# Performance work log

Measured on AMD Instinct MI355X. Metric: run time of the kernel, lower is better.

The kernel has to match this reference:

```python
import jax, jax.numpy as jnp
import numpy as np
from functools import partial


def deform_sample(inp, dy, dx):
    """Bilinear sample inp[b,c] at (y+dy[b,c,y,x], x+dx[b,c,y,x]) with zero padding.
    inp, dy, dx: [B, C, H, W] -> [B, C, H, W]. Matches torchvision deform_conv2d
    with 1x1 kernel and offset_groups == C (one offset pair per channel)."""
    B, C, H, W = inp.shape
    ys = jnp.arange(H, dtype=inp.dtype)[None, None, :, None] + dy  # [B,C,H,W]
    xs = jnp.arange(W, dtype=inp.dtype)[None, None, None, :] + dx
    y0f = jnp.floor(ys)
    x0f = jnp.floor(xs)
    wy = ys - y0f
    wx = xs - x0f
    y0 = y0f.astype(jnp.int32)
    x0 = x0f.astype(jnp.int32)
    flat = inp.reshape(B, C, H * W)

    def gather(yi, xi):
        valid = (yi >= 0) & (yi < H) & (xi >= 0) & (xi < W)
        idx = jnp.clip(yi, 0, H - 1) * W + jnp.clip(xi, 0, W - 1)
        v = jnp.take_along_axis(flat, idx.reshape(B, C, H * W), axis=2).reshape(B, C, H, W)
        return jnp.where(valid, v, jnp.zeros((), inp.dtype))

    return ((1 - wy) * (1 - wx) * gather(y0, x0)
            + (1 - wy) * wx * gather(y0, x0 + 1)
            + wy * (1 - wx) * gather(y0 + 1, x0)
            + wy * wx * gather(y0 + 1, x0 + 1))


def atm_layer(x, offset, w_weight, w_bias, h_weight, h_bias, local_weight, local_bias,
              fc1_w, fc1_b, fc2_w, fc2_b, proj_w, proj_b):
    B, H, W, C = x.shape
    x_nchw = jnp.transpose(x, (0, 3, 1, 2))  # [B,C,H,W]
    zeros = jnp.zeros_like(x_nchw)

    # ATM along w: offset[:, :C] is x-offset (offset_t[:,1::2]), y-offset 0
    sw = deform_sample(x_nchw, zeros, offset[:, :C])
    w = jnp.einsum('bchw,oc->bhwo', sw, w_weight) + w_bias  # [B,H,W,C]

    # ATM along h: offset[:, C:] is y-offset (offset_t[:,0::2]), x-offset 0
    sh = deform_sample(x_nchw, offset[:, C:], zeros)
    h = jnp.einsum('bchw,oc->bhwo', sh, h_weight) + h_bias

    # depthwise 5x5 conv, padding 2
    c = jax.lax.conv_general_dilated(
        x_nchw, local_weight, window_strides=(1, 1), padding=((2, 2), (2, 2)),
        feature_group_count=C, dimension_numbers=('NCHW', 'OIHW', 'NCHW'))
    c = jnp.transpose(c, (0, 2, 3, 1)) + local_bias  # [B,H,W,C]

    # gating MLP: global average -> fc1 -> GELU -> fc2 -> softmax over 3 branches
    a = (w + h + c).mean(axis=(1, 2))  # [B,C]
    a = jax.nn.gelu(a @ fc1_w.T + fc1_b, approximate=False)
    a = a @ fc2_w.T + fc2_b  # [B,3C]
    a = jnp.transpose(a.reshape(B, C, 3), (2, 0, 1))  # [3,B,C]
    a = jax.nn.softmax(a, axis=0)[:, :, None, None, :]  # [3,B,1,1,C]

    out = w * a[0] + h * a[1] + c * a[2]
    out = out @ proj_w.T + proj_b
    return out


def setup_inputs() -> dict:
    C = 256
    B, H, W = 16, 64, 64
    key = jax.random.key(0)
    ks = jax.random.split(key, 16)
    bnd = 1.0 / np.sqrt(C)
    hid = C // 4
    return {
        'x': jax.random.normal(ks[0], (B, H, W, C), jnp.float32),
        'offset': jax.random.normal(ks[1], (B, 2 * C, H, W), jnp.float32),
        'w_weight': jax.random.uniform(ks[2], (C, C), jnp.float32, -bnd, bnd),
        'w_bias': jax.random.uniform(ks[3], (C,), jnp.float32, -bnd, bnd),
        'h_weight': jax.random.uniform(ks[4], (C, C), jnp.float32, -bnd, bnd),
        'h_bias': jax.random.uniform(ks[5], (C,), jnp.float32, -bnd, bnd),
        'local_weight': jax.random.uniform(ks[6], (C, 1, 5, 5), jnp.float32, -0.2, 0.2),
        'local_bias': jax.random.uniform(ks[7], (C,), jnp.float32, -0.2, 0.2),
        'fc1_w': jax.random.uniform(ks[8], (hid, C), jnp.float32, -bnd, bnd),
        'fc1_b': jax.random.uniform(ks[9], (hid,), jnp.float32, -bnd, bnd),
        'fc2_w': jax.random.uniform(ks[10], (3 * C, hid), jnp.float32, -1.0 / np.sqrt(hid), 1.0 / np.sqrt(hid)),
        'fc2_b': jax.random.uniform(ks[11], (3 * C,), jnp.float32, -1.0 / np.sqrt(hid), 1.0 / np.sqrt(hid)),
        'proj_w': jax.random.uniform(ks[12], (C, C), jnp.float32, -bnd, bnd),
        'proj_b': jax.random.uniform(ks[13], (C,), jnp.float32, -bnd, bnd),
    }


def reference(x, offset, w_weight, w_bias, h_weight, h_bias, local_weight, local_bias,
              fc1_w, fc1_b, fc2_w, fc2_b, proj_w, proj_b):
    return atm_layer(x, offset, w_weight, w_bias, h_weight, h_bias, local_weight,
                     local_bias, fc1_w, fc1_b, fc2_w, fc2_b, proj_w, proj_b)
```

## Files before the change

kernel.cpp:

```cpp
#include <hip/hip_runtime.h>
#include <hip/hip_bf16.h>

typedef _Float16 half4_t __attribute__((ext_vector_type(4)));
typedef _Float16 half8 __attribute__((ext_vector_type(8)));
typedef float f32x4 __attribute__((ext_vector_type(4)));

#define BB 16
#define HH 64
#define WW2 64
#define CC 256

__global__ __launch_bounds__(256) void k_pre(
    const float* __restrict__ Ww, const float* __restrict__ Wh,
    const float* __restrict__ pw,
    _Float16* __restrict__ WwT, _Float16* __restrict__ WhT,
    _Float16* __restrict__ pf, float* __restrict__ sums)
{
  __shared__ _Float16 tile[64][65];
  const int blk = blockIdx.x;
  const int t = threadIdx.x;

  if (blk < 32) {
    const int nt = blk & 3, kt = (blk >> 2) & 3, mat = blk >> 4;
    const float* src = mat ? Wh : Ww;
    _Float16* dst = mat ? WhT : WwT;
    const int n0 = nt * 64, k0 = kt * 64;
    const int sl = t & 63;
    #pragma unroll
    for (int p = 0; p < 16; p++) {
      int chl = (t >> 6) + p * 4;
      tile[chl][sl] = (_Float16)src[(size_t)(n0 + chl) * 256 + k0 + sl];
    }
    __syncthreads();
    #pragma unroll
    for (int p = 0; p < 2; p++) {
      int pl = (t >> 3) + p * 32;
      int c8 = (t & 7) * 8;
      half8 hv;
      #pragma unroll
      for (int r = 0; r < 8; r++) hv[r] = tile[c8 + r][pl];
      *(half8*)(dst + (size_t)(k0 + pl) * 256 + n0 + c8) = hv;
    }
  } else if (blk < 80) {
    sums[(blk - 32) * 256 + t] = 0.f;
  } else {
    int i = (blk - 80) * 2048 + t * 8;
    float4 v0 = *(const float4*)(pw + i);
    float4 v1 = *(const float4*)(pw + i + 4);
    half8 h = {(_Float16)v0.x, (_Float16)v0.y, (_Float16)v0.z, (_Float16)v0.w,
               (_Float16)v1.x, (_Float16)v1.y, (_Float16)v1.z, (_Float16)v1.w};
    *(half8*)(pf + i) = h;
  }
}

__global__ __launch_bounds__(256) void k_transA(
    const float* __restrict__ x, const float* __restrict__ off,
    _Float16* __restrict__ swb, float* __restrict__ ssw)
{
  __shared__ _Float16 tile[64][65];
  __shared__ _Float16 xr[64][68];
  __shared__ float red[4][64];

  const int work = (blockIdx.x & 7) * 512 + (blockIdx.x >> 3);
  const int st   = work & 63;
  const int cht  = (work >> 6) & 3;
  const int b    = work >> 8;
  const int t = threadIdx.x;

  const int ch0 = cht * 64;
  const float* src = off + ((size_t)b * 512 + ch0) * 4096 + st * 64;
  const int sl = t & 63;
  #pragma unroll
  for (int p = 0; p < 16; p++) {
    int chl = (t >> 6) + p * 4;
    tile[chl][sl] = (_Float16)src[(size_t)chl * 4096 + sl];
  }

  const float* xs_src = x + ((size_t)(b * 64 + st) * 64) * 256 + ch0;
  const int xrow = t >> 2;
  const int c16 = (t & 3) * 16;
  #pragma unroll
  for (int j = 0; j < 4; j++) {
    float4 v = *(const float4*)(xs_src + (size_t)xrow * 256 + c16 + j * 4);
    half4_t h = {(_Float16)v.x, (_Float16)v.y, (_Float16)v.z, (_Float16)v.w};
    *(half4_t*)(&xr[xrow][c16 + j * 4]) = h;
  }
  __syncthreads();

  const int cl = t & 63, xg = t >> 6;
  const int cg = ch0 + cl;
  _Float16* sp = swb + ((size_t)(b * 64 + st) * 64) * 256 + cg;
  float asw = 0.f;
  #pragma unroll
  for (int k = 0; k < 16; k++) {
    int xi = xg * 16 + k;
    float dx = (float)tile[cl][xi];
    float xs2 = (float)xi + dx;
    float xf = floorf(xs2);
    float wx = xs2 - xf;
    int xq = (int)xf;
    float v0 = (xq >= 0 && xq < 64) ? (float)xr[xq][cl] : 0.f;
    float v1 = (xq + 1 >= 0 && xq + 1 < 64) ? (float)xr[xq + 1][cl] : 0.f;
    float swv = (1.f - wx) * v0 + wx * v1;
    sp[(size_t)xi * 256] = (_Float16)swv;
    asw += swv;
  }
  red[xg][cl] = asw;
  __syncthreads();
  if (t < 64)
    atomicAdd(&ssw[b * CC + ch0 + t],
              red[0][t] + red[1][t] + red[2][t] + red[3][t]);
}

__global__ __launch_bounds__(256) void k_transB(const float* __restrict__ off,
                                                _Float16* __restrict__ offBT)
{
  __shared__ _Float16 tile[64][65];
  const int work = (blockIdx.x & 7) * 512 + (blockIdx.x >> 3);
  const int st   = work & 63;
  const int cht  = (work >> 6) & 3;
  const int b    = work >> 8;
  const int t = threadIdx.x;

  const int ch0 = 256 + cht * 64;
  const float* src = off + ((size_t)b * 512 + ch0) * 4096 + st * 64;
  const int sl = t & 63;
  #pragma unroll
  for (int p = 0; p < 16; p++) {
    int chl = (t >> 6) + p * 4;
    tile[chl][sl] = (_Float16)src[(size_t)chl * 4096 + sl];
  }
  __syncthreads();

  #pragma unroll
  for (int p = 0; p < 2; p++) {
    int pl = (t >> 3) + p * 32;
    int c8 = (t & 7) * 8;
    half8 hv;
    #pragma unroll
    for (int r = 0; r < 8; r++) hv[r] = tile[c8 + r][pl];
    int s = st * 64 + pl;
    size_t pix = (size_t)b * 4096 + (s & 63) * 64 + (s >> 6);
    *(half8*)(offBT + pix * 256 + cht * 64 + c8) = hv;
  }
}

__global__ __launch_bounds__(256) void k_conv(
    const float* __restrict__ x, const float* __restrict__ lw,
    _Float16* __restrict__ cvb, float* __restrict__ scv)
{
  const int work = (blockIdx.x & 7) * 256 + (blockIdx.x >> 3);
  const int xh = work & 1;
  const int y  = (work >> 1) & 63;
  const int b  = work >> 7;
  const int c = threadIdx.x;

  float wgt[25];
  #pragma unroll
  for (int q = 0; q < 25; q++) wgt[q] = lw[c * 25 + q];

  const float* xb = x + (size_t)b * HH * WW2 * CC + c;
  const float* rp[5];
  bool yv[5];
  #pragma unroll
  for (int ky = 0; ky < 5; ky++) {
    int yy = y + ky - 2;
    yv[ky] = (yy >= 0 && yy < HH);
    rp[ky] = xb + (size_t)(yv[ky] ? yy : 0) * WW2 * CC;
  }

  _Float16* cp = cvb + ((size_t)b * 4096 + y * 64) * CC + c;
  float acv = 0.f;
  const int x0 = xh * 32;

  for (int g = 0; g < 4; ++g) {
    const int u0 = x0 + g * 8;
    float col[60];
    #pragma unroll
    for (int j = 0; j < 12; j++) {
      int xx = u0 + j - 2;
      bool xv = (xx >= 0 && xx < 64);
      int xxc = xv ? xx : 0;
      #pragma unroll
      for (int ky = 0; ky < 5; ky++) {
        float v = rp[ky][(size_t)xxc * CC];
        col[j * 5 + ky] = (xv && yv[ky]) ? v : 0.f;
      }
    }
    #pragma unroll
    for (int o = 0; o < 8; o++) {
      float cv = 0.f;
      #pragma unroll
      for (int kx = 0; kx < 5; kx++) {
        const int j5 = (o + kx) * 5;
        cv += wgt[0 + kx]  * col[j5 + 0] + wgt[5 + kx]  * col[j5 + 1] +
              wgt[10 + kx] * col[j5 + 2] + wgt[15 + kx] * col[j5 + 3] +
              wgt[20 + kx] * col[j5 + 4];
      }
      cp[(size_t)(u0 + o) * CC] = (_Float16)cv;
      acv += cv;
    }
  }
  atomicAdd(&scv[b * CC + c], acv);
}

__global__ __launch_bounds__(256) void k_col(
    const float* __restrict__ x, const _Float16* __restrict__ offBT,
    _Float16* __restrict__ shb, float* __restrict__ ssh)
{
  __shared__ _Float16 xc[64 * 128];
  const int work = (blockIdx.x & 7) * 256 + (blockIdx.x >> 3);
  const int ch = work & 1;
  const int xi = (work >> 1) & 63;
  const int b  = work >> 7;
  const int ch0 = ch * 128;
  const int t = threadIdx.x;

  #pragma unroll
  for (int p = 0; p < 4; p++) {
    int i = p * 2048 + t * 8;
    int yy = i >> 7, cl = i & 127;
    const float* s = x + ((size_t)(b * 64 + yy) * 64 + xi) * 256 + ch0 + cl;
    float4 v0 = *(const float4*)(s);
    float4 v1 = *(const float4*)(s + 4);
    half8 h = {(_Float16)v0.x, (_Float16)v0.y, (_Float16)v0.z, (_Float16)v0.w,
               (_Float16)v1.x, (_Float16)v1.y, (_Float16)v1.z, (_Float16)v1.w};
    *(half8*)(xc + i) = h;
  }
  __syncthreads();

  const int cl = t & 127, yg = t >> 7;
  const _Float16* obt = offBT + ((size_t)(b * 64 + xi) * 64) * 256 + ch0 + cl;
  _Float16* hp = shb + ((size_t)(b * 64) * 64 + xi) * 256 + ch0 + cl;
  float ash = 0.f;
  #pragma unroll 8
  for (int k = 0; k < 32; k++) {
    int yy = yg * 32 + k;
    float dy = (float)obt[(size_t)yy * 256];
    float ys = (float)yy + dy;
    float yf = floorf(ys);
    float wy = ys - yf;
    int yq = (int)yf;
    float u0 = (yq >= 0 && yq < 64) ? (float)xc[yq * 128 + cl] : 0.f;
    float u1 = (yq + 1 >= 0 && yq + 1 < 64) ? (float)xc[(yq + 1) * 128 + cl] : 0.f;
    float shv = (1.f - wy) * u0 + wy * u1;
    hp[(size_t)yy * 64 * 256] = (_Float16)shv;
    ash += shv;
  }
  atomicAdd(&ssh[b * CC + ch0 + cl], ash);
}

__global__ __launch_bounds__(256) void k_gate(
    const float* __restrict__ ssw, const float* __restrict__ ssh, const float* __restrict__ scv,
    const float* __restrict__ Ww, const float* __restrict__ bw,
    const float* __restrict__ Wh, const float* __restrict__ bh,
    const float* __restrict__ blc,
    const float* __restrict__ fc1w, const float* __restrict__ fc1b,
    const float* __restrict__ fc2w, const float* __restrict__ fc2b,
    _Float16* __restrict__ gh, float* __restrict__ bcomb)
{
  __shared__ float sswl[CC], sshl[CC], avgl[CC], tl[64];
  const int b = blockIdx.x, tid = threadIdx.x;
  sswl[tid] = ssw[b * CC + tid];
  sshl[tid] = ssh[b * CC + tid];
  __syncthreads();

  float acc = scv[b * CC + tid];
  for (int c = 0; c < CC; c++)
    acc += sswl[c] * Ww[tid * CC + c] + sshl[c] * Wh[tid * CC + c];
  avgl[tid] = acc * (1.f / (HH * WW2)) + bw[tid] + bh[tid] + blc[tid];
  __syncthreads();

  if (tid < 64) {
    float a = fc1b[tid];
    for (int o = 0; o < CC; o++) a += avgl[o] * fc1w[tid * CC + o];
    tl[tid] = 0.5f * a * (1.f + erff(a * 0.70710678118654752f));
  }
  __syncthreads();

  float g[3];
  #pragma unroll
  for (int j = 0; j < 3; j++) {
    float a = fc2b[tid * 3 + j];
    for (int k = 0; k < 64; k++) a += tl[k] * fc2w[(tid * 3 + j) * 64 + k];
    g[j] = a;
  }
  float m = fmaxf(g[0], fmaxf(g[1], g[2]));
  float e0 = expf(g[0] - m), e1 = expf(g[1] - m), e2 = expf(g[2] - m);
  float inv = 1.f / (e0 + e1 + e2);
  float a0 = e0 * inv, a1 = e1 * inv, a2 = e2 * inv;
  gh[(0 * BB + b) * CC + tid] = (_Float16)a0;
  gh[(1 * BB + b) * CC + tid] = (_Float16)a1;
  gh[(2 * BB + b) * CC + tid] = (_Float16)a2;
  bcomb[b * CC + tid] = a0 * bw[tid] + a1 * bh[tid] + a2 * blc[tid];
}

__global__ __launch_bounds__(256) void k_mats(
    const _Float16* __restrict__ pf, const _Float16* __restrict__ gh,
    const _Float16* __restrict__ WwT, const _Float16* __restrict__ WhT,
    const float* __restrict__ bcomb, const float* __restrict__ pb,
    _Float16* __restrict__ Bcat, float* __restrict__ bias_out)
{
  const int blk = (blockIdx.x & 7) * 16 + (blockIdx.x >> 3);
  const int ob = blk & 3;
  const int br = (blk >> 2) & 1;
  const int b  = blk >> 3;
  const int o0 = ob * 64;
  const int tid = threadIdx.x;
  const int wid = tid >> 6, l = tid & 63;
  const int n0 = wid * 64;
  const int lr = l & 15;
  const int kg = (l >> 4) * 8;
  const int jr = (l >> 4) * 4;

  const _Float16* WT  = br ? WhT : WwT;
  const _Float16* ghb = gh + (size_t)(br * BB + b) * CC;

  f32x4 acc[4][4];
  #pragma unroll
  for (int mi = 0; mi < 4; mi++)
    #pragma unroll
    for (int ni = 0; ni < 4; ni++) acc[mi][ni] = (f32x4){0.f, 0.f, 0.f, 0.f};

  #pragma unroll
  for (int ks = 0; ks < 8; ks++) {
    half8 gv = *(const half8*)(ghb + kg + ks * 32);
    half8 a[4], bbv[4];
    #pragma unroll
    for (int mi = 0; mi < 4; mi++)
      a[mi] = *(const half8*)(pf + (size_t)(o0 + mi * 16 + lr) * CC + kg + ks * 32) * gv;
    #pragma unroll
    for (int ni = 0; ni < 4; ni++)
      bbv[ni] = *(const half8*)(WT + (size_t)(n0 + ni * 16 + lr) * CC + kg + ks * 32);
    #pragma unroll
    for (int mi = 0; mi < 4; mi++)
      #pragma unroll
      for (int ni = 0; ni < 4; ni++)
        acc[mi][ni] = __builtin_amdgcn_mfma_f32_16x16x32_f16(a[mi], bbv[ni], acc[mi][ni], 0, 0, 0);
  }

  #pragma unroll
  for (int ni = 0; ni < 4; ni++) {
    int kcol = n0 + ni * 16 + lr;
    #pragma unroll
    for (int mi = 0; mi < 4; mi++) {
      #pragma unroll
      for (int j = 0; j < 4; j++) {
        int o = o0 + mi * 16 + jr + j;
        Bcat[((size_t)b * CC + o) * 512 + br * 256 + kcol] = (_Float16)acc[mi][ni][j];
      }
    }
  }

  if (br == 0) {
    int o_l = tid >> 2, part = tid & 3;
    const _Float16* pr = pf + (size_t)(o0 + o_l) * CC + part * 64;
    const float* bc = bcomb + b * CC + part * 64;
    float s = 0.f;
    #pragma unroll
    for (int i = 0; i < 8; i++) {
      half8 h = *(const half8*)(pr + i * 8);
      #pragma unroll
      for (int r = 0; r < 8; r++) s += (float)h[r] * bc[i * 8 + r];
    }
    s += __shfl_xor(s, 1);
    s += __shfl_xor(s, 2);
    if (part == 0) bias_out[b * CC + o0 + o_l] = s + pb[o0 + o_l];
  }
}

#define APAD 264
__global__ __launch_bounds__(256) void k_gemm(
    const _Float16* __restrict__ swb, const _Float16* __restrict__ shb,
    const _Float16* __restrict__ cvb, const _Float16* __restrict__ Bcat,
    const _Float16* __restrict__ pf, const _Float16* __restrict__ a2h,
    const float* __restrict__ bias_out, float* __restrict__ out)
{
  __shared__ _Float16 smem[64 * APAD];

  const int work = (blockIdx.x & 7) * 128 + (blockIdx.x >> 3);
  const int r0 = work * 64;
  const int b = work >> 6;
  const int tid = threadIdx.x;
  const int wid = tid >> 6, l = tid & 63;
  const int n0 = wid * 64;
  const int lr = l & 15;
  const int kg = (l >> 4) * 8;
  const int jr = (l >> 4) * 4;

  const _Float16* bq = Bcat + ((size_t)b * CC + n0 + lr) * 512 + kg;

  f32x4 acc[4][4];
  #pragma unroll
  for (int mi = 0; mi < 4; mi++)
    #pragma unroll
    for (int ni = 0; ni < 4; ni++) acc[mi][ni] = (f32x4){0.f, 0.f, 0.f, 0.f};

  half8 st[8];
  {
    const _Float16* g = swb + (size_t)r0 * CC;
    #pragma unroll
    for (int p = 0; p < 8; p++) st[p] = *(const half8*)(g + p * 2048 + tid * 8);
    #pragma unroll
    for (int p = 0; p < 8; p++) {
      int i = p * 2048 + tid * 8;
      *(half8*)(smem + (i >> 8) * APAD + (i & 255)) = st[p];
    }
  }
  __syncthreads();
  {
    const _Float16* g = shb + (size_t)r0 * CC;
    #pragma unroll
    for (int p = 0; p < 8; p++) st[p] = *(const half8*)(g + p * 2048 + tid * 8);
  }
  #pragma unroll
  for (int ks = 0; ks < 8; ks++) {
    half8 a[4], bbv[4];
    #pragma unroll
    for (int mi = 0; mi < 4; mi++)
      a[mi] = *(const half8*)(smem + (mi * 16 + lr) * APAD + kg + ks * 32);
    #pragma unroll
    for (int ni = 0; ni < 4; ni++)
      bbv[ni] = *(const half8*)(bq + (size_t)ni * 16 * 512 + ks * 32);
    #pragma unroll
    for (int mi = 0; mi < 4; mi++)
      #pragma unroll
      for (int ni = 0; ni < 4; ni++)
        acc[mi][ni] = __builtin_amdgcn_mfma_f32_16x16x32_f16(a[mi], bbv[ni], acc[mi][ni], 0, 0, 0);
  }
  __syncthreads();
  #pragma unroll
  for (int p = 0; p < 8; p++) {
    int i = p * 2048 + tid * 8;
    *(half8*)(smem + (i >> 8) * APAD + (i & 255)) = st[p];
  }
  __syncthreads();
  {
    const _Float16* g = cvb + (size_t)r0 * CC;
    #pragma unroll
    for (int p = 0; p < 8; p++) st[p] = *(const half8*)(g + p * 2048 + tid * 8);
  }
  #pragma unroll
  for (int ks = 0; ks < 8; ks++) {
    half8 a[4], bbv[4];
    #pragma unroll
    for (int mi = 0; mi < 4; mi++)
      a[mi] = *(const half8*)(smem + (mi * 16 + lr) * APAD + kg + ks * 32);
    #pragma unroll
    for (int ni = 0; ni < 4; ni++)
      bbv[ni] = *(const half8*)(bq + (size_t)ni * 16 * 512 + 256 + ks * 32);
    #pragma unroll
    for (int mi = 0; mi < 4; mi++)
      #pragma unroll
      for (int ni = 0; ni < 4; ni++)
        acc[mi][ni] = __builtin_amdgcn_mfma_f32_16x16x32_f16(a[mi], bbv[ni], acc[mi][ni], 0, 0, 0);
  }
  __syncthreads();
  #pragma unroll
  for (int p = 0; p < 8; p++) {
    int i = p * 2048 + tid * 8;
    *(half8*)(smem + (i >> 8) * APAD + (i & 255)) = st[p];
  }
  __syncthreads();
  const _Float16* a2b = a2h + (size_t)b * CC;
  #pragma unroll
  for (int ks = 0; ks < 8; ks++) {
    half8 a2v = *(const half8*)(a2b + kg + ks * 32);
    half8 a[4], bbv[4];
    #pragma unroll
    for (int mi = 0; mi < 4; mi++)
      a[mi] = *(const half8*)(smem + (mi * 16 + lr) * APAD + kg + ks * 32);
    #pragma unroll
    for (int ni = 0; ni < 4; ni++)
      bbv[ni] = *(const half8*)(pf + (size_t)(n0 + ni * 16 + lr) * CC + kg + ks * 32) * a2v;
    #pragma unroll
    for (int mi = 0; mi < 4; mi++)
      #pragma unroll
      for (int ni = 0; ni < 4; ni++)
        acc[mi][ni] = __builtin_amdgcn_mfma_f32_16x16x32_f16(a[mi], bbv[ni], acc[mi][ni], 0, 0, 0);
  }

  #pragma unroll
  for (int ni = 0; ni < 4; ni++) {
    int col = n0 + ni * 16 + lr;
    float bo = bias_out[b * CC + col];
    #pragma unroll
    for (int mi = 0; mi < 4; mi++) {
      #pragma unroll
      for (int j = 0; j < 4; j++) {
        size_t idx = (size_t)(r0 + mi * 16 + jr + j) * CC + col;
        out[idx] = acc[mi][ni][j] + bo;
      }
    }
  }
}

extern "C" void kernel_launch(void* const* d_in, const int* in_sizes, int n_in,
                              void* d_out, int out_size, void* d_ws, size_t ws_size,
                              hipStream_t stream)
{
  const float* x    = (const float*)d_in[0];
  const float* off  = (const float*)d_in[1];
  const float* Ww   = (const float*)d_in[2];
  const float* bw   = (const float*)d_in[3];
  const float* Wh   = (const float*)d_in[4];
  const float* bh   = (const float*)d_in[5];
  const float* lw   = (const float*)d_in[6];
  const float* blc  = (const float*)d_in[7];
  const float* fc1w = (const float*)d_in[8];
  const float* fc1b = (const float*)d_in[9];
  const float* fc2w = (const float*)d_in[10];
  const float* fc2b = (const float*)d_in[11];
  const float* pw   = (const float*)d_in[12];
  const float* pb   = (const float*)d_in[13];
  float* out = (float*)d_out;

  char* ws = (char*)d_ws;
  _Float16* shb   = (_Float16*)(ws + 0);
  _Float16* cvb   = (_Float16*)(ws + 33554432);
  _Float16* offBT = (_Float16*)(ws + 67108864);
  _Float16* swb   = (_Float16*)(ws + 100663296);
  _Float16* Bcat  = (_Float16*)(ws + 134217728);
  _Float16* pf    = (_Float16*)(ws + 138412032);
  _Float16* gh    = (_Float16*)(ws + 138543104);
  float* bcomb    = (float*)(ws + 138567680);
  float* bias_out = (float*)(ws + 138584064);
  _Float16* WwT = (_Float16*)((char*)d_out + 0);
  _Float16* WhT = (_Float16*)((char*)d_out + 131072);
  float* sums   = (float*)((char*)d_out + 262144);
  float* ssw = sums, *ssh = sums + 4096, *scv = sums + 8192;

  k_pre<<<112, 256, 0, stream>>>(Ww, Wh, pw, WwT, WhT, pf, sums);
  k_transB<<<4096, 256, 0, stream>>>(off, offBT);
  k_col<<<2048, 256, 0, stream>>>(x, offBT, shb, ssh);
  k_transA<<<4096, 256, 0, stream>>>(x, off, swb, ssw);
  k_conv<<<2048, 256, 0, stream>>>(x, lw, cvb, scv);
  k_gate<<<BB, 256, 0, stream>>>(ssw, ssh, scv, Ww, bw, Wh, bh, blc,
                                 fc1w, fc1b, fc2w, fc2b, gh, bcomb);
  k_mats<<<128, 256, 0, stream>>>(pf, gh, WwT, WhT, bcomb, pb, Bcat, bias_out);
  k_gemm<<<1024, 256, 0, stream>>>(swb, shb, cvb, Bcat, pf, gh + 2 * BB * CC,
                                   bias_out, out);
}
```

Measured before the change: 256.2 us.

## Fuse staging kernels, replace ssw atomics with partials, double-buffer GEMM LDS

```diff
diff --git a/kernel.cpp b/kernel.cpp
--- a/kernel.cpp
+++ b/kernel.cpp
@@ -10,18 +10,95 @@
 #define WW2 64
 #define CC 256
 
-__global__ __launch_bounds__(256) void k_pre(
+__global__ __launch_bounds__(256) void k_stage(
+    const float* __restrict__ x, const float* __restrict__ off,
     const float* __restrict__ Ww, const float* __restrict__ Wh,
     const float* __restrict__ pw,
+    _Float16* __restrict__ swb, _Float16* __restrict__ offBT,
     _Float16* __restrict__ WwT, _Float16* __restrict__ WhT,
-    _Float16* __restrict__ pf, float* __restrict__ sums)
+    _Float16* __restrict__ pf,
+    float* __restrict__ sswp, float* __restrict__ zbase)
 {
   __shared__ _Float16 tile[64][65];
-  const int blk = blockIdx.x;
+  __shared__ _Float16 xr[64][68];
+  __shared__ float red[4][64];
+
+  const int work = (blockIdx.x & 7) * 1036 + (blockIdx.x >> 3);
   const int t = threadIdx.x;
 
-  if (blk < 32) {
-    const int nt = blk & 3, kt = (blk >> 2) & 3, mat = blk >> 4;
+  if (work < 4096) {
+    const int st   = work & 63;
+    const int cht  = (work >> 6) & 3;
+    const int b    = work >> 8;
+    const int ch0 = cht * 64;
+    const float* src = off + ((size_t)b * 512 + ch0) * 4096 + st * 64;
+    const int sl = t & 63;
+    #pragma unroll
+    for (int p = 0; p < 16; p++) {
+      int chl = (t >> 6) + p * 4;
+      tile[chl][sl] = (_Float16)src[(size_t)chl * 4096 + sl];
+    }
+    const float* xs_src = x + ((size_t)(b * 64 + st) * 64) * 256 + ch0;
+    const int xrow = t >> 2;
+    const int c16 = (t & 3) * 16;
+    #pragma unroll
+    for (int j = 0; j < 4; j++) {
+      float4 v = *(const float4*)(xs_src + (size_t)xrow * 256 + c16 + j * 4);
+      half4_t h = {(_Float16)v.x, (_Float16)v.y, (_Float16)v.z, (_Float16)v.w};
+      *(half4_t*)(&xr[xrow][c16 + j * 4]) = h;
+    }
+    __syncthreads();
+
+    const int cl = t & 63, xg = t >> 6;
+    _Float16* sp = swb + ((size_t)(b * 64 + st) * 64) * 256 + ch0 + cl;
+    float asw = 0.f;
+    #pragma unroll
+    for (int k = 0; k < 16; k++) {
+      int xi = xg * 16 + k;
+      float dx = (float)tile[cl][xi];
+      float xs2 = (float)xi + dx;
+      float xf = floorf(xs2);
+      float wx = xs2 - xf;
+      int xq = (int)xf;
+      float v0 = (xq >= 0 && xq < 64) ? (float)xr[xq][cl] : 0.f;
+      float v1 = (xq + 1 >= 0 && xq + 1 < 64) ? (float)xr[xq + 1][cl] : 0.f;
+      float swv = (1.f - wx) * v0 + wx * v1;
+      sp[(size_t)xi * 256] = (_Float16)swv;
+      asw += swv;
+    }
+    red[xg][cl] = asw;
+    __syncthreads();
+    if (t < 64)
+      sswp[((size_t)(b * 64 + st)) * 256 + ch0 + t] =
+          red[0][t] + red[1][t] + red[2][t] + red[3][t];
+  } else if (work < 8192) {
+    const int w2 = work - 4096;
+    const int st   = w2 & 63;
+    const int cht  = (w2 >> 6) & 3;
+    const int b    = w2 >> 8;
+    const int ch0 = 256 + cht * 64;
+    const float* src = off + ((size_t)b * 512 + ch0) * 4096 + st * 64;
+    const int sl = t & 63;
+    #pragma unroll
+    for (int p = 0; p < 16; p++) {
+      int chl = (t >> 6) + p * 4;
+      tile[chl][sl] = (_Float16)src[(size_t)chl * 4096 + sl];
+    }
+    __syncthreads();
+    #pragma unroll
+    for (int p = 0; p < 2; p++) {
+      int pl = (t >> 3) + p * 32;
+      int c8 = (t & 7) * 8;
+      half8 hv;
+      #pragma unroll
+      for (int r = 0; r < 8; r++) hv[r] = tile[c8 + r][pl];
+      int s = st * 64 + pl;
+      size_t pix = (size_t)b * 4096 + (s & 63) * 64 + (s >> 6);
+      *(half8*)(offBT + pix * 256 + cht * 64 + c8) = hv;
+    }
+  } else if (work < 8224) {
+    const int w3 = work - 8192;
+    const int nt = w3 & 3, kt = (w3 >> 2) & 3, mat = w3 >> 4;
     const float* src = mat ? Wh : Ww;
     _Float16* dst = mat ? WhT : WwT;
     const int n0 = nt * 64, k0 = kt * 64;
@@ -41,107 +118,15 @@
       for (int r = 0; r < 8; r++) hv[r] = tile[c8 + r][pl];
       *(half8*)(dst + (size_t)(k0 + pl) * 256 + n0 + c8) = hv;
     }
-  } else if (blk < 80) {
-    sums[(blk - 32) * 256 + t] = 0.f;
-  } else {
-    int i = (blk - 80) * 2048 + t * 8;
+  } else if (work < 8256) {
+    int i = (work - 8224) * 2048 + t * 8;
     float4 v0 = *(const float4*)(pw + i);
     float4 v1 = *(const float4*)(pw + i + 4);
     half8 h = {(_Float16)v0.x, (_Float16)v0.y, (_Float16)v0.z, (_Float16)v0.w,
                (_Float16)v1.x, (_Float16)v1.y, (_Float16)v1.z, (_Float16)v1.w};
     *(half8*)(pf + i) = h;
-  }
-}
-
-__global__ __launch_bounds__(256) void k_transA(
-    const float* __restrict__ x, const float* __restrict__ off,
-    _Float16* __restrict__ swb, float* __restrict__ ssw)
-{
-  __shared__ _Float16 tile[64][65];
-  __shared__ _Float16 xr[64][68];
-  __shared__ float red[4][64];
-
-  const int work = (blockIdx.x & 7) * 512 + (blockIdx.x >> 3);
-  const int st   = work & 63;
-  const int cht  = (work >> 6) & 3;
-  const int b    = work >> 8;
-  const int t = threadIdx.x;
-
-  const int ch0 = cht * 64;
-  const float* src = off + ((size_t)b * 512 + ch0) * 4096 + st * 64;
-  const int sl = t & 63;
-  #pragma unroll
-  for (int p = 0; p < 16; p++) {
-    int chl = (t >> 6) + p * 4;
-    tile[chl][sl] = (_Float16)src[(size_t)chl * 4096 + sl];
-  }
-
-  const float* xs_src = x + ((size_t)(b * 64 + st) * 64) * 256 + ch0;
-  const int xrow = t >> 2;
-  const int c16 = (t & 3) * 16;
-  #pragma unroll
-  for (int j = 0; j < 4; j++) {
-    float4 v = *(const float4*)(xs_src + (size_t)xrow * 256 + c16 + j * 4);
-    half4_t h = {(_Float16)v.x, (_Float16)v.y, (_Float16)v.z, (_Float16)v.w};
-    *(half4_t*)(&xr[xrow][c16 + j * 4]) = h;
-  }
-  __syncthreads();
-
-  const int cl = t & 63, xg = t >> 6;
-  const int cg = ch0 + cl;
-  _Float16* sp = swb + ((size_t)(b * 64 + st) * 64) * 256 + cg;
-  float asw = 0.f;
-  #pragma unroll
-  for (int k = 0; k < 16; k++) {
-    int xi = xg * 16 + k;
-    float dx = (float)tile[cl][xi];
-    float xs2 = (float)xi + dx;
-    float xf = floorf(xs2);
-    float wx = xs2 - xf;
-    int xq = (int)xf;
-    float v0 = (xq >= 0 && xq < 64) ? (float)xr[xq][cl] : 0.f;
-    float v1 = (xq + 1 >= 0 && xq + 1 < 64) ? (float)xr[xq + 1][cl] : 0.f;
-    float swv = (1.f - wx) * v0 + wx * v1;
-    sp[(size_t)xi * 256] = (_Float16)swv;
-    asw += swv;
-  }
-  red[xg][cl] = asw;
-  __syncthreads();
-  if (t < 64)
-    atomicAdd(&ssw[b * CC + ch0 + t],
-              red[0][t] + red[1][t] + red[2][t] + red[3][t]);
-}
-
-__global__ __launch_bounds__(256) void k_transB(const float* __restrict__ off,
-                                                _Float16* __restrict__ offBT)
-{
-  __shared__ _Float16 tile[64][65];
-  const int work = (blockIdx.x & 7) * 512 + (blockIdx.x >> 3);
-  const int st   = work & 63;
-  const int cht  = (work >> 6) & 3;
-  const int b    = work >> 8;
-  const int t = threadIdx.x;
-
-  const int ch0 = 256 + cht * 64;
-  const float* src = off + ((size_t)b * 512 + ch0) * 4096 + st * 64;
-  const int sl = t & 63;
-  #pragma unroll
-  for (int p = 0; p < 16; p++) {
-    int chl = (t >> 6) + p * 4;
-    tile[chl][sl] = (_Float16)src[(size_t)chl * 4096 + sl];
-  }
-  __syncthreads();
-
-  #pragma unroll
-  for (int p = 0; p < 2; p++) {
-    int pl = (t >> 3) + p * 32;
-    int c8 = (t & 7) * 8;
-    half8 hv;
-    #pragma unroll
-    for (int r = 0; r < 8; r++) hv[r] = tile[c8 + r][pl];
-    int s = st * 64 + pl;
-    size_t pix = (size_t)b * 4096 + (s & 63) * 64 + (s >> 6);
-    *(half8*)(offBT + pix * 256 + cht * 64 + c8) = hv;
+  } else {
+    zbase[(work - 8256) * 256 + t] = 0.f;
   }
 }
 
@@ -251,7 +236,8 @@
 }
 
 __global__ __launch_bounds__(256) void k_gate(
-    const float* __restrict__ ssw, const float* __restrict__ ssh, const float* __restrict__ scv,
+    const float* __restrict__ sswp, const float* __restrict__ ssh,
+    const float* __restrict__ scv,
     const float* __restrict__ Ww, const float* __restrict__ bw,
     const float* __restrict__ Wh, const float* __restrict__ bh,
     const float* __restrict__ blc,
@@ -261,7 +247,11 @@
 {
   __shared__ float sswl[CC], sshl[CC], avgl[CC], tl[64];
   const int b = blockIdx.x, tid = threadIdx.x;
-  sswl[tid] = ssw[b * CC + tid];
+
+  float s_sw = 0.f;
+  for (int q = 0; q < 64; q++)
+    s_sw += sswp[((size_t)(b * 64 + q)) * 256 + tid];
+  sswl[tid] = s_sw;
   sshl[tid] = ssh[b * CC + tid];
   __syncthreads();
 
@@ -376,7 +366,9 @@
     const _Float16* __restrict__ pf, const _Float16* __restrict__ a2h,
     const float* __restrict__ bias_out, float* __restrict__ out)
 {
-  __shared__ _Float16 smem[64 * APAD];
+  __shared__ _Float16 smem[2 * 64 * APAD];
+  _Float16* buf0 = smem;
+  _Float16* buf1 = smem + 64 * APAD;
 
   const int work = (blockIdx.x & 7) * 128 + (blockIdx.x >> 3);
   const int r0 = work * 64;
@@ -404,7 +396,7 @@
     #pragma unroll
     for (int p = 0; p < 8; p++) {
       int i = p * 2048 + tid * 8;
-      *(half8*)(smem + (i >> 8) * APAD + (i & 255)) = st[p];
+      *(half8*)(buf0 + (i >> 8) * APAD + (i & 255)) = st[p];
     }
   }
   __syncthreads();
@@ -418,7 +410,7 @@
     half8 a[4], bbv[4];
     #pragma unroll
     for (int mi = 0; mi < 4; mi++)
-      a[mi] = *(const half8*)(smem + (mi * 16 + lr) * APAD + kg + ks * 32);
+      a[mi] = *(const half8*)(buf0 + (mi * 16 + lr) * APAD + kg + ks * 32);
     #pragma unroll
     for (int ni = 0; ni < 4; ni++)
       bbv[ni] = *(const half8*)(bq + (size_t)ni * 16 * 512 + ks * 32);
@@ -428,11 +420,10 @@
       for (int ni = 0; ni < 4; ni++)
         acc[mi][ni] = __builtin_amdgcn_mfma_f32_16x16x32_f16(a[mi], bbv[ni], acc[mi][ni], 0, 0, 0);
   }
-  __syncthreads();
   #pragma unroll
   for (int p = 0; p < 8; p++) {
     int i = p * 2048 + tid * 8;
-    *(half8*)(smem + (i >> 8) * APAD + (i & 255)) = st[p];
+    *(half8*)(buf1 + (i >> 8) * APAD + (i & 255)) = st[p];
   }
   __syncthreads();
   {
@@ -445,7 +436,7 @@
     half8 a[4], bbv[4];
     #pragma unroll
     for (int mi = 0; mi < 4; mi++)
-      a[mi] = *(const half8*)(smem + (mi * 16 + lr) * APAD + kg + ks * 32);
+      a[mi] = *(const half8*)(buf1 + (mi * 16 + lr) * APAD + kg + ks * 32);
     #pragma unroll
     for (int ni = 0; ni < 4; ni++)
       bbv[ni] = *(const half8*)(bq + (size_t)ni * 16 * 512 + 256 + ks * 32);
@@ -455,11 +446,10 @@
       for (int ni = 0; ni < 4; ni++)
         acc[mi][ni] = __builtin_amdgcn_mfma_f32_16x16x32_f16(a[mi], bbv[ni], acc[mi][ni], 0, 0, 0);
   }
-  __syncthreads();
   #pragma unroll
   for (int p = 0; p < 8; p++) {
     int i = p * 2048 + tid * 8;
-    *(half8*)(smem + (i >> 8) * APAD + (i & 255)) = st[p];
+    *(half8*)(buf0 + (i >> 8) * APAD + (i & 255)) = st[p];
   }
   __syncthreads();
   const _Float16* a2b = a2h + (size_t)b * CC;
@@ -469,7 +459,7 @@
     half8 a[4], bbv[4];
     #pragma unroll
     for (int mi = 0; mi < 4; mi++)
-      a[mi] = *(const half8*)(smem + (mi * 16 + lr) * APAD + kg + ks * 32);
+      a[mi] = *(const half8*)(buf0 + (mi * 16 + lr) * APAD + kg + ks * 32);
     #pragma unroll
     for (int ni = 0; ni < 4; ni++)
       bbv[ni] = *(const half8*)(pf + (size_t)(n0 + ni * 16 + lr) * CC + kg + ks * 32) * a2v;
@@ -528,14 +518,15 @@
   _Float16* WwT = (_Float16*)((char*)d_out + 0);
   _Float16* WhT = (_Float16*)((char*)d_out + 131072);
   float* sums   = (float*)((char*)d_out + 262144);
-  float* ssw = sums, *ssh = sums + 4096, *scv = sums + 8192;
-
-  k_pre<<<112, 256, 0, stream>>>(Ww, Wh, pw, WwT, WhT, pf, sums);
-  k_transB<<<4096, 256, 0, stream>>>(off, offBT);
+  float* sswp   = (float*)((char*)d_out + 311296);
+  float* ssh = sums + 4096, *scv = sums + 8192;
+
+  k_stage<<<8288, 256, 0, stream>>>(x, off, Ww, Wh, pw,
+                                    swb, offBT, WwT, WhT, pf,
+                                    sswp, ssh );
   k_col<<<2048, 256, 0, stream>>>(x, offBT, shb, ssh);
-  k_transA<<<4096, 256, 0, stream>>>(x, off, swb, ssw);
   k_conv<<<2048, 256, 0, stream>>>(x, lw, cvb, scv);
-  k_gate<<<BB, 256, 0, stream>>>(ssw, ssh, scv, Ww, bw, Wh, bh, blc,
+  k_gate<<<BB, 256, 0, stream>>>(sswp, ssh, scv, Ww, bw, Wh, bh, blc,
                                  fc1w, fc1b, fc2w, fc2b, gh, bcomb);
   k_mats<<<128, 256, 0, stream>>>(pf, gh, WwT, WhT, bcomb, pb, Bcat, bias_out);
   k_gemm<<<1024, 256, 0, stream>>>(swb, shb, cvb, Bcat, pf, gh + 2 * BB * CC,
```

Result: faster. 246.7 us (-3.7%).
